# Performance work log

Hardware: AMD Instinct MI355X
Metric: run time of the kernel (lower is better)

Reference implementation:

```python
import jax, jax.numpy as jnp
import numpy as np

B, S, DQK, DV, H = 4, 2048, 128, 128, 8


def setup_inputs() -> dict:
    key = jax.random.key(0)
    ks = jax.random.split(key, 9)
    s = 0.02
    return {
        "query": jax.random.normal(ks[0], (B, S, DQK), jnp.float32),
        "key": jax.random.normal(ks[1], (B, S, DQK), jnp.float32),
        "value": jax.random.normal(ks[2], (B, S, DV), jnp.float32),
        "WQ": jax.random.normal(ks[3], (DQK, H * DQK), jnp.float32) * s,
        "bQ": jax.random.normal(ks[4], (H * DQK,), jnp.float32) * s,
        "WK": jax.random.normal(ks[5], (DQK, H * DQK), jnp.float32) * s,
        "bK": jax.random.normal(ks[6], (H * DQK,), jnp.float32) * s,
        "WV": jax.random.normal(ks[7], (DV, H * DV), jnp.float32) * s,
        "bV": jax.random.normal(ks[8], (H * DV,), jnp.float32) * s,
    }


def reference(query, key, value, WQ, bQ, WK, bK, WV, bV):
    b, qn, dqk = query.shape
    kn = key.shape[1]
    dv = value.shape[2]
    h = H
    # projections -> [b, n, h, d]
    Q = (query @ WQ + bQ).reshape(b, qn, h, dqk)
    K = (key @ WK + bK).reshape(b, kn, h, dqk)
    V = (value @ WV + bV).reshape(b, kn, h, dv)
    # abs(QK^T)/sqrt(dk) score -- non-standard, prevents flash kernels
    scores = jnp.abs(jnp.einsum("bqhd,bkhd->bhqk", Q, K)) / jnp.sqrt(
        jnp.asarray(dqk, query.dtype)
    )
    w = jax.nn.softmax(scores, axis=-1)  # [b,h,q,k]
    # (complex cast +0j in the original is numerically a no-op on real V)
    out = jnp.einsum("bhqk,bkhd->bqhd", w, V).reshape(b, qn, h * dv)
    return out
```

## Files before the change

kernel.cpp:

```cpp
#include <hip/hip_runtime.h>
#include <hip/hip_bf16.h>

#define B_ 4
#define S_ 2048
#define D_ 128
#define H_ 8

typedef __attribute__((ext_vector_type(8))) short bf16x8;
typedef __attribute__((ext_vector_type(4))) float f32x4;

__device__ __forceinline__ short f2bf(float f) {
  union { float f; unsigned u; } v; v.f = f;
  unsigned u = v.u;
  unsigned r = (u + 0x7FFFu + ((u >> 16) & 1u)) >> 16;
  return (short)r;
}

__device__ __forceinline__ short4 pack4(f32x4 p) {
  union { __hip_bfloat162 h2[2]; short4 s4; } u;
  u.h2[0] = __float22bfloat162_rn(make_float2(p[0], p[1]));
  u.h2[1] = __float22bfloat162_rn(make_float2(p[2], p[3]));
  return u.s4;
}

__device__ __forceinline__ void dma16(const short* g, short* l) {
  __builtin_amdgcn_global_load_lds(
      (const __attribute__((address_space(1))) unsigned int*)g,
      (__attribute__((address_space(3))) unsigned int*)l, 16, 0, 0);
}

__global__ __launch_bounds__(256) void prep(
    const float* __restrict__ WQ, const float* __restrict__ WK, const float* __restrict__ WV,
    short* __restrict__ TQ, short* __restrict__ TK, short* __restrict__ TV) {
  __shared__ float tile[64][65];
  int bw = blockIdx.x >> 5;
  int tl = blockIdx.x & 31;
  int n0 = (tl & 15) * 64, k0 = (tl >> 4) * 64;
  const float* W = (bw == 0) ? WQ : (bw == 1) ? WK : WV;
  short* Wt = (bw == 0) ? TQ : (bw == 1) ? TK : TV;
#pragma unroll
  for (int i = 0; i < 16; ++i) {
    int cix = threadIdx.x + 256 * i;
    int rr = cix >> 6, cc = cix & 63;
    tile[rr][cc] = W[(k0 + rr) * 1024 + n0 + cc];
  }
  __syncthreads();
#pragma unroll
  for (int i = 0; i < 16; ++i) {
    int cix = threadIdx.x + 256 * i;
    int rr = cix >> 6, cc = cix & 63;
    Wt[(n0 + rr) * 128 + k0 + cc] = f2bf(tile[cc][rr]);
  }
}

template <int WA>
__device__ __forceinline__ void proj_tile(const float* __restrict__ X,
                                          const short* __restrict__ Wt,
                                          const float* __restrict__ bias,
                                          short* __restrict__ out,
                                          int mtile, int ntile,
                                          short* sA, short* sB) {
  int tid = threadIdx.x;
  int lane = tid & 63, w = tid >> 6;
  int l15 = lane & 15, l4 = lane >> 4;
  int m0 = mtile * 128, n0 = ntile * 128;

#pragma unroll
  for (int j = 0; j < 8; ++j) {
    int f = w * 8 + j;
    const short* src = Wt + (n0 + (f >> 2) * 16 + l15) * 128 + (f & 3) * 32 + l4 * 8;
    dma16(src, sB + f * 512);
  }
#pragma unroll
  for (int j = 0; j < 8; ++j) {
    int f = w * 8 + j;
    const float* src = X + (size_t)(m0 + (f >> 2) * 16 + l15) * 128 + (f & 3) * 32 + l4 * 8;
    float4 v0 = *(const float4*)src;
    float4 v1 = *(const float4*)(src + 4);
    union { struct { short4 lo, hi; } s; bf16x8 v; } u;
    u.s.lo = pack4((f32x4){v0.x, v0.y, v0.z, v0.w});
    u.s.hi = pack4((f32x4){v1.x, v1.y, v1.z, v1.w});
    *(bf16x8*)(sA + f * 512 + lane * 8) = u.v;
  }
  __syncthreads();

  int wr = w >> 1, wc = w & 1;
  f32x4 acc[4][4];
#pragma unroll
  for (int mi = 0; mi < 4; ++mi)
#pragma unroll
    for (int ni = 0; ni < 4; ++ni) acc[mi][ni] = (f32x4){0.f, 0.f, 0.f, 0.f};

#pragma unroll
  for (int mi = 0; mi < 4; ++mi) {
    bf16x8 a[4];
#pragma unroll
    for (int st = 0; st < 4; ++st)
      a[st] = *(const bf16x8*)(sA + ((wr * 4 + mi) * 4 + st) * 512 + lane * 8);
#pragma unroll
    for (int ni = 0; ni < 4; ++ni) {
#pragma unroll
      for (int st = 0; st < 4; ++st) {
        bf16x8 b = *(const bf16x8*)(sB + ((wc * 4 + ni) * 4 + st) * 512 + lane * 8);
        if (WA)
          acc[mi][ni] = __builtin_amdgcn_mfma_f32_16x16x32_bf16(b, a[st], acc[mi][ni], 0, 0, 0);
        else
          acc[mi][ni] = __builtin_amdgcn_mfma_f32_16x16x32_bf16(a[st], b, acc[mi][ni], 0, 0, 0);
      }
    }
  }

  if (WA) {
#pragma unroll
    for (int mi = 0; mi < 4; ++mi) {
      int sg = m0 + wr * 64 + mi * 16 + l15;
      int bb = sg >> 11, s = sg & 2047;
      short* orow = out + ((size_t)(bb * H_ + ntile) * S_ + s) * D_;
#pragma unroll
      for (int ni = 0; ni < 4; ++ni) {
        int d0 = wc * 64 + ni * 16 + l4 * 4;
        float4 bv = *(const float4*)(bias + n0 + d0);
        f32x4 t = acc[mi][ni];
        t[0] += bv.x; t[1] += bv.y; t[2] += bv.z; t[3] += bv.w;
        *(short4*)(orow + d0) = pack4(t);
      }
    }
  } else {
#pragma unroll
    for (int ni = 0; ni < 4; ++ni) {
      int d = wc * 64 + ni * 16 + l15;
      float bvs = bias[n0 + d];
#pragma unroll
      for (int mi = 0; mi < 4; ++mi) {
        int sg0 = m0 + wr * 64 + mi * 16 + l4 * 4;
        int bb = sg0 >> 11, s0 = sg0 & 2047;
        f32x4 t = acc[mi][ni];
        t[0] += bvs; t[1] += bvs; t[2] += bvs; t[3] += bvs;
        size_t off = (size_t)(bb * H_ + ntile) * (S_ * D_)
                   + (size_t)(s0 >> 6) * 8192
                   + (size_t)((d >> 4) * 2 + ((s0 >> 5) & 1)) * 512
                   + ((s0 >> 3) & 3) * 128 + (d & 15) * 8
                   + (s0 & 7);
        *(short4*)(out + off) = pack4(t);
      }
    }
  }
}

__global__ __launch_bounds__(256, 2) void proj3(
    const float* __restrict__ xq, const float* __restrict__ xk, const float* __restrict__ xv,
    const short* __restrict__ wtq, const short* __restrict__ wtk, const short* __restrict__ wtv,
    const float* __restrict__ bQ, const float* __restrict__ bK, const float* __restrict__ bV,
    short* __restrict__ Qp, short* __restrict__ Kp, short* __restrict__ Vf) {
  __shared__ short sA[16384], sB[16384];
  int work = (blockIdx.x & 7) * 192 + (blockIdx.x >> 3);
  int which = work >> 9;
  int t = work & 511;
  int mtile = t >> 3, ntile = t & 7;
  if (which == 0)      proj_tile<1>(xq, wtq, bQ, Qp, mtile, ntile, sA, sB);
  else if (which == 1) proj_tile<1>(xk, wtk, bK, Kp, mtile, ntile, sA, sB);
  else                 proj_tile<0>(xv, wtv, bV, Vf, mtile, ntile, sA, sB);
}

#define BN 64
#define PSTR 72

#define KDMA(BUF, T)                                                           \
  {                                                                            \
    const short* kgs = kg + (T) * BN * D_;                                     \
    short* kl = (BUF) + (w * 4) * 512;                                         \
    dma16(kgs, kl);                                                            \
    dma16(kgs + 32, kl + 512);                                                 \
    dma16(kgs + 64, kl + 1024);                                                \
    dma16(kgs + 96, kl + 1536);                                                \
  }

#define QK_CLUSTER(KB)                                                         \
  _Pragma("unroll") for (int mt = 0; mt < 4; ++mt) {                           \
    s0[mt] = (f32x4){0.f, 0.f, 0.f, 0.f};                                      \
    s1[mt] = (f32x4){0.f, 0.f, 0.f, 0.f};                                      \
    _Pragma("unroll") for (int st = 0; st < 4; ++st) {                         \
      bf16x8 bk = *(const bf16x8*)((KB) + (mt * 4 + st) * 512 + lane * 8);     \
      s0[mt] = __builtin_amdgcn_mfma_f32_16x16x32_bf16(bk, aq[0][st], s0[mt], 0, 0, 0); \
      s1[mt] = __builtin_amdgcn_mfma_f32_16x16x32_bf16(bk, aq[1][st], s1[mt], 0, 0, 0); \
    }                                                                          \
  }

#define SM_CLUSTER()                                                           \
  _Pragma("unroll") for (int mt = 0; mt < 4; ++mt) {                           \
    _Pragma("unroll") for (int r = 0; r < 4; ++r) {                            \
      float p = __builtin_amdgcn_exp2f(fabsf(s0[mt][r]) * SC2);                \
      ls0 += p;                                                                \
      s0[mt][r] = p;                                                           \
    }                                                                          \
    *(short4*)(pw + l15 * PSTR + mt * 16 + l4 * 4) = pack4(s0[mt]);            \
  }                                                                            \
  ap0[0] = *(const bf16x8*)(pw + l15 * PSTR + l4 * 8);                         \
  ap0[1] = *(const bf16x8*)(pw + l15 * PSTR + 32 + l4 * 8);                    \
  _Pragma("unroll") for (int mt = 0; mt < 4; ++mt) {                           \
    _Pragma("unroll") for (int r = 0; r < 4; ++r) {                            \
      float p = __builtin_amdgcn_exp2f(fabsf(s1[mt][r]) * SC2);                \
      ls1 += p;                                                                \
      s1[mt][r] = p;                                                           \
    }                                                                          \
    *(short4*)(pw + l15 * PSTR + mt * 16 + l4 * 4) = pack4(s1[mt]);            \
  }                                                                            \
  ap1[0] = *(const bf16x8*)(pw + l15 * PSTR + l4 * 8);                         \
  ap1[1] = *(const bf16x8*)(pw + l15 * PSTR + 32 + l4 * 8);

#define PV_CLUSTER()                                                           \
  _Pragma("unroll") for (int t8 = 0; t8 < 8; ++t8) {                           \
    _Pragma("unroll") for (int kst = 0; kst < 2; ++kst) {                      \
      o0[t8] = __builtin_amdgcn_mfma_f32_16x16x32_bf16(ap0[kst], bv[t8 * 2 + kst], o0[t8], 0, 0, 0); \
      o1[t8] = __builtin_amdgcn_mfma_f32_16x16x32_bf16(ap1[kst], bv[t8 * 2 + kst], o1[t8], 0, 0, 0); \
    }                                                                          \
  }

__global__ __launch_bounds__(256, 2) void attn(const short* __restrict__ Qp,
                                               const short* __restrict__ Kp,
                                               const short* __restrict__ Vf,
                                               float* __restrict__ out) {
  __shared__ short sK0[8192], sK1[8192];
  __shared__ short sP[4 * 16 * PSTR];

  int tid = threadIdx.x;
  int lane = tid & 63, w = tid >> 6;
  int swz = (blockIdx.x & 7) * 64 + (blockIdx.x >> 3);
  int qt = swz & 15;
  int bh = swz >> 4;
  int q0 = qt * 128;
  int l15 = lane & 15, l4 = lane >> 4;

  const short* Qbase = Qp + (size_t)bh * S_ * D_;
  const short* Kbase = Kp + (size_t)bh * S_ * D_;
  const short* vfb = Vf + (size_t)bh * S_ * D_ + lane * 8;

  const short* kg = Kbase + (w * 16 + l15) * D_ + l4 * 8;

  KDMA(sK0, 0);

  bf16x8 aq[2][4];
#pragma unroll
  for (int g = 0; g < 2; ++g)
#pragma unroll
    for (int st = 0; st < 4; ++st)
      aq[g][st] = *(const bf16x8*)(Qbase + (q0 + w * 32 + g * 16 + l15) * D_ + l4 * 8 + 32 * st);

  f32x4 o0[8], o1[8];
#pragma unroll
  for (int t = 0; t < 8; ++t) {
    o0[t] = (f32x4){0.f, 0.f, 0.f, 0.f};
    o1[t] = (f32x4){0.f, 0.f, 0.f, 0.f};
  }
  float ls0 = 0.f, ls1 = 0.f;

  const float SC2 = 0.127530637f;
  short* pw = sP + w * 16 * PSTR;

  __syncthreads();

  f32x4 s0[4], s1[4];
  bf16x8 ap0[2], ap1[2];

  KDMA(sK1, 1);
  QK_CLUSTER(sK0);
  SM_CLUSTER();
  __syncthreads();

  for (int t = 0; t < 31; ++t) {
    bf16x8 bv[16];
#pragma unroll
    for (int f = 0; f < 16; ++f)
      bv[f] = *(const bf16x8*)(vfb + t * 8192 + f * 512);
    __builtin_amdgcn_sched_barrier(0);
    if (t < 30) {
      short* kdst = (t & 1) ? sK1 : sK0;
      KDMA(kdst, t + 2);
    }
    const short* kb = (t & 1) ? sK0 : sK1;
    __builtin_amdgcn_s_setprio(1);
    QK_CLUSTER(kb);
    PV_CLUSTER();
    __builtin_amdgcn_s_setprio(0);
    SM_CLUSTER();
    __syncthreads();
  }

  {
    bf16x8 bv[16];
#pragma unroll
    for (int f = 0; f < 16; ++f)
      bv[f] = *(const bf16x8*)(vfb + 31 * 8192 + f * 512);
    PV_CLUSTER();
  }

  ls0 += __shfl_xor(ls0, 16);
  ls0 += __shfl_xor(ls0, 32);
  ls1 += __shfl_xor(ls1, 16);
  ls1 += __shfl_xor(ls1, 32);
  float inv0[4], inv1[4];
#pragma unroll
  for (int r = 0; r < 4; ++r) {
    inv0[r] = 1.f / __shfl(ls0, l4 * 4 + r);
    inv1[r] = 1.f / __shfl(ls1, l4 * 4 + r);
  }

  int bb = bh >> 3, h = bh & 7;
#pragma unroll
  for (int t = 0; t < 8; ++t) {
#pragma unroll
    for (int r = 0; r < 4; ++r) {
      int qA = q0 + w * 32 + l4 * 4 + r;
      int qB = qA + 16;
      out[((size_t)(bb * S_ + qA)) * (H_ * D_) + h * D_ + t * 16 + l15] = o0[t][r] * inv0[r];
      out[((size_t)(bb * S_ + qB)) * (H_ * D_) + h * D_ + t * 16 + l15] = o1[t][r] * inv1[r];
    }
  }
}

extern "C" void kernel_launch(void* const* d_in, const int* in_sizes, int n_in,
                              void* d_out, int out_size, void* d_ws, size_t ws_size,
                              hipStream_t stream) {
  (void)in_sizes; (void)n_in; (void)out_size; (void)ws_size;
  const float* q  = (const float*)d_in[0];
  const float* k  = (const float*)d_in[1];
  const float* v  = (const float*)d_in[2];
  const float* WQ = (const float*)d_in[3];
  const float* bQ = (const float*)d_in[4];
  const float* WK = (const float*)d_in[5];
  const float* bK = (const float*)d_in[6];
  const float* WV = (const float*)d_in[7];
  const float* bV = (const float*)d_in[8];

  const int NW = D_ * H_ * D_;
  const int NP = B_ * H_ * S_ * D_;

  short* ws  = (short*)d_ws;
  short* wtq = ws;
  short* wtk = wtq + NW;
  short* wtv = wtk + NW;
  short* Qp  = wtv + NW;
  short* Kp  = Qp + NP;
  short* Vf  = Kp + NP;

  prep<<<96, 256, 0, stream>>>(WQ, WK, WV, wtq, wtk, wtv);

  proj3<<<1536, 256, 0, stream>>>(q, k, v, wtq, wtk, wtv, bQ, bK, bV, Qp, Kp, Vf);

  attn<<<512, 256, 0, stream>>>(Qp, Kp, Vf, (float*)d_out);
}
```

Before: 196.5 us.

## Store K in MFMA fragment layout and load it directly to registers

```diff
diff --git a/kernel.cpp b/kernel.cpp
--- a/kernel.cpp
+++ b/kernel.cpp
@@ -53,7 +53,7 @@
   }
 }
 
-template <int WA>
+template <int MODE>
 __device__ __forceinline__ void proj_tile(const float* __restrict__ X,
                                           const short* __restrict__ Wt,
                                           const float* __restrict__ bias,
@@ -102,7 +102,7 @@
 #pragma unroll
       for (int st = 0; st < 4; ++st) {
         bf16x8 b = *(const bf16x8*)(sB + ((wc * 4 + ni) * 4 + st) * 512 + lane * 8);
-        if (WA)
+        if (MODE <= 1)
           acc[mi][ni] = __builtin_amdgcn_mfma_f32_16x16x32_bf16(b, a[st], acc[mi][ni], 0, 0, 0);
         else
           acc[mi][ni] = __builtin_amdgcn_mfma_f32_16x16x32_bf16(a[st], b, acc[mi][ni], 0, 0, 0);
@@ -110,7 +110,7 @@
     }
   }
 
-  if (WA) {
+  if (MODE == 0) {
 #pragma unroll
     for (int mi = 0; mi < 4; ++mi) {
       int sg = m0 + wr * 64 + mi * 16 + l15;
@@ -123,6 +123,23 @@
         f32x4 t = acc[mi][ni];
         t[0] += bv.x; t[1] += bv.y; t[2] += bv.z; t[3] += bv.w;
         *(short4*)(orow + d0) = pack4(t);
+      }
+    }
+  } else if (MODE == 1) {
+#pragma unroll
+    for (int mi = 0; mi < 4; ++mi) {
+      int key = m0 + wr * 64 + mi * 16 + l15;
+      int bb = key >> 11, k = key & 2047;
+      size_t base = (size_t)(bb * H_ + ntile) * (S_ * D_) + (size_t)(k >> 6) * 8192
+                  + ((k >> 4) & 3) * 4 * 512 + (k & 15) * 8;
+#pragma unroll
+      for (int ni = 0; ni < 4; ++ni) {
+        int d0 = wc * 64 + ni * 16 + l4 * 4;
+        float4 bv = *(const float4*)(bias + n0 + d0);
+        f32x4 t = acc[mi][ni];
+        t[0] += bv.x; t[1] += bv.y; t[2] += bv.z; t[3] += bv.w;
+        size_t off = base + (size_t)(d0 >> 5) * 512 + ((d0 >> 3) & 3) * 128 + (d0 & 7);
+        *(short4*)(out + off) = pack4(t);
       }
     }
   } else {
@@ -147,42 +164,30 @@
   }
 }
 
-__global__ __launch_bounds__(256, 2) void proj3(
+__global__ __launch_bounds__(256, 3) void proj3(
     const float* __restrict__ xq, const float* __restrict__ xk, const float* __restrict__ xv,
     const short* __restrict__ wtq, const short* __restrict__ wtk, const short* __restrict__ wtv,
     const float* __restrict__ bQ, const float* __restrict__ bK, const float* __restrict__ bV,
-    short* __restrict__ Qp, short* __restrict__ Kp, short* __restrict__ Vf) {
+    short* __restrict__ Qp, short* __restrict__ Kf, short* __restrict__ Vf) {
   __shared__ short sA[16384], sB[16384];
   int work = (blockIdx.x & 7) * 192 + (blockIdx.x >> 3);
   int which = work >> 9;
   int t = work & 511;
   int mtile = t >> 3, ntile = t & 7;
-  if (which == 0)      proj_tile<1>(xq, wtq, bQ, Qp, mtile, ntile, sA, sB);
-  else if (which == 1) proj_tile<1>(xk, wtk, bK, Kp, mtile, ntile, sA, sB);
-  else                 proj_tile<0>(xv, wtv, bV, Vf, mtile, ntile, sA, sB);
-}
-
-#define BN 64
+  if (which == 0)      proj_tile<0>(xq, wtq, bQ, Qp, mtile, ntile, sA, sB);
+  else if (which == 1) proj_tile<1>(xk, wtk, bK, Kf, mtile, ntile, sA, sB);
+  else                 proj_tile<2>(xv, wtv, bV, Vf, mtile, ntile, sA, sB);
+}
+
 #define PSTR 72
 
-#define KDMA(BUF, T)                                                           \
-  {                                                                            \
-    const short* kgs = kg + (T) * BN * D_;                                     \
-    short* kl = (BUF) + (w * 4) * 512;                                         \
-    dma16(kgs, kl);                                                            \
-    dma16(kgs + 32, kl + 512);                                                 \
-    dma16(kgs + 64, kl + 1024);                                                \
-    dma16(kgs + 96, kl + 1536);                                                \
-  }
-
-#define QK_CLUSTER(KB)                                                         \
+#define QK_CLUSTER()                                                           \
   _Pragma("unroll") for (int mt = 0; mt < 4; ++mt) {                           \
     s0[mt] = (f32x4){0.f, 0.f, 0.f, 0.f};                                      \
     s1[mt] = (f32x4){0.f, 0.f, 0.f, 0.f};                                      \
     _Pragma("unroll") for (int st = 0; st < 4; ++st) {                         \
-      bf16x8 bk = *(const bf16x8*)((KB) + (mt * 4 + st) * 512 + lane * 8);     \
-      s0[mt] = __builtin_amdgcn_mfma_f32_16x16x32_bf16(bk, aq[0][st], s0[mt], 0, 0, 0); \
-      s1[mt] = __builtin_amdgcn_mfma_f32_16x16x32_bf16(bk, aq[1][st], s1[mt], 0, 0, 0); \
+      s0[mt] = __builtin_amdgcn_mfma_f32_16x16x32_bf16(kf[mt * 4 + st], aq[0][st], s0[mt], 0, 0, 0); \
+      s1[mt] = __builtin_amdgcn_mfma_f32_16x16x32_bf16(kf[mt * 4 + st], aq[1][st], s1[mt], 0, 0, 0); \
     }                                                                          \
   }
 
@@ -217,10 +222,9 @@
   }
 
 __global__ __launch_bounds__(256, 2) void attn(const short* __restrict__ Qp,
-                                               const short* __restrict__ Kp,
+                                               const short* __restrict__ Kf,
                                                const short* __restrict__ Vf,
                                                float* __restrict__ out) {
-  __shared__ short sK0[8192], sK1[8192];
   __shared__ short sP[4 * 16 * PSTR];
 
   int tid = threadIdx.x;
@@ -232,12 +236,8 @@
   int l15 = lane & 15, l4 = lane >> 4;
 
   const short* Qbase = Qp + (size_t)bh * S_ * D_;
-  const short* Kbase = Kp + (size_t)bh * S_ * D_;
+  const short* kfb = Kf + (size_t)bh * S_ * D_ + lane * 8;
   const short* vfb = Vf + (size_t)bh * S_ * D_ + lane * 8;
-
-  const short* kg = Kbase + (w * 16 + l15) * D_ + l4 * 8;
-
-  KDMA(sK0, 0);
 
   bf16x8 aq[2][4];
 #pragma unroll
@@ -257,41 +257,26 @@
   const float SC2 = 0.127530637f;
   short* pw = sP + w * 16 * PSTR;
 
-  __syncthreads();
-
-  f32x4 s0[4], s1[4];
-  bf16x8 ap0[2], ap1[2];
-
-  KDMA(sK1, 1);
-  QK_CLUSTER(sK0);
-  SM_CLUSTER();
-  __syncthreads();
-
-  for (int t = 0; t < 31; ++t) {
+  for (int t = 0; t < S_ / 64; ++t) {
+    bf16x8 kf[16];
+#pragma unroll
+    for (int f = 0; f < 16; ++f)
+      kf[f] = *(const bf16x8*)(kfb + t * 8192 + f * 512);
     bf16x8 bv[16];
 #pragma unroll
     for (int f = 0; f < 16; ++f)
       bv[f] = *(const bf16x8*)(vfb + t * 8192 + f * 512);
     __builtin_amdgcn_sched_barrier(0);
-    if (t < 30) {
-      short* kdst = (t & 1) ? sK1 : sK0;
-      KDMA(kdst, t + 2);
-    }
-    const short* kb = (t & 1) ? sK0 : sK1;
+
+    f32x4 s0[4], s1[4];
     __builtin_amdgcn_s_setprio(1);
-    QK_CLUSTER(kb);
+    QK_CLUSTER();
+    __builtin_amdgcn_s_setprio(0);
+    bf16x8 ap0[2], ap1[2];
+    SM_CLUSTER();
+    __builtin_amdgcn_s_setprio(1);
     PV_CLUSTER();
     __builtin_amdgcn_s_setprio(0);
-    SM_CLUSTER();
-    __syncthreads();
-  }
-
-  {
-    bf16x8 bv[16];
-#pragma unroll
-    for (int f = 0; f < 16; ++f)
-      bv[f] = *(const bf16x8*)(vfb + 31 * 8192 + f * 512);
-    PV_CLUSTER();
   }
 
   ls0 += __shfl_xor(ls0, 16);
@@ -340,12 +325,12 @@
   short* wtk = wtq + NW;
   short* wtv = wtk + NW;
   short* Qp  = wtv + NW;
-  short* Kp  = Qp + NP;
-  short* Vf  = Kp + NP;
+  short* Kf  = Qp + NP;
+  short* Vf  = Kf + NP;
 
   prep<<<96, 256, 0, stream>>>(WQ, WK, WV, wtq, wtk, wtv);
 
-  proj3<<<1536, 256, 0, stream>>>(q, k, v, wtq, wtk, wtv, bQ, bK, bV, Qp, Kp, Vf);
-
-  attn<<<512, 256, 0, stream>>>(Qp, Kp, Vf, (float*)d_out);
-}
+  proj3<<<1536, 256, 0, stream>>>(q, k, v, wtq, wtk, wtv, bQ, bK, bV, Qp, Kf, Vf);
+
+  attn<<<512, 256, 0, stream>>>(Qp, Kf, Vf, (float*)d_out);
+}
```

New measurement: 194.8 us. No clear change (-0.9%).
